# Kernel tuning notes

Hardware: AMD Instinct MI355X
Metric: run time of the kernel (lower is better)

Reference implementation:

```python
import jax, jax.numpy as jnp
import numpy as np

N_GRIDS, N_FEATS = 64, 2
GD = GH = GW = 64
PE_TERMS, N_DIMS = 6, 3
NODES, N_OUT = 64, 1
N_PTS = 524288


def setup_inputs() -> dict:
    key = jax.random.key(0)
    ks = jax.random.split(key, 8)
    x = jax.random.uniform(ks[0], (N_PTS, N_DIMS), jnp.float32, -1.0, 1.0)
    grid_scales = jax.random.uniform(ks[1], (N_GRIDS, 3), jnp.float32, 1.0, 4.0)
    grid_translations = jax.random.uniform(ks[2], (N_GRIDS, 3), jnp.float32, -1.0, 1.0) * (grid_scales - 1.0)
    feature_grids = jax.random.normal(ks[3], (N_GRIDS, N_FEATS, GD, GH, GW), jnp.float32)
    d_in = PE_TERMS * N_DIMS * 2 + N_FEATS * N_GRIDS  # 36 + 128 = 164
    W0 = jax.random.normal(ks[4], (d_in, NODES), jnp.float32) * np.sqrt(2.0 / (d_in + NODES))
    b0 = jnp.zeros((NODES,), jnp.float32)
    W1 = jax.random.normal(ks[5], (NODES, NODES), jnp.float32) * np.sqrt(2.0 / (2 * NODES))
    b1 = jnp.zeros((NODES,), jnp.float32)
    W2 = jax.random.normal(ks[6], (NODES, N_OUT), jnp.float32) * np.sqrt(2.0 / (NODES + N_OUT))
    b2 = jnp.zeros((N_OUT,), jnp.float32)
    return dict(x=x, grid_scales=grid_scales, grid_translations=grid_translations,
                feature_grids=feature_grids, W0=W0, b0=b0, W1=W1, b1=b1, W2=W2, b2=b2)


def grid_sample_3d(vol, coords):
    """Trilinear grid_sample, align_corners=True, padding_mode='zeros'.
    vol: [C,D,H,W]; coords: [N,3] in (x,y,z) order (x -> W axis), range [-1,1].
    Returns [C,N]."""
    C, D, H, W = vol.shape
    flat = vol.reshape(C, D * H * W)
    ix = (coords[:, 0] + 1.0) * 0.5 * (W - 1)
    iy = (coords[:, 1] + 1.0) * 0.5 * (H - 1)
    iz = (coords[:, 2] + 1.0) * 0.5 * (D - 1)
    x0 = jnp.floor(ix); y0 = jnp.floor(iy); z0 = jnp.floor(iz)
    wx = ix - x0; wy = iy - y0; wz = iz - z0
    x0i = x0.astype(jnp.int32); y0i = y0.astype(jnp.int32); z0i = z0.astype(jnp.int32)
    out = jnp.zeros((C, coords.shape[0]), vol.dtype)
    for dz, wz_ in ((0, 1.0 - wz), (1, wz)):
        for dy, wy_ in ((0, 1.0 - wy), (1, wy)):
            for dx, wx_ in ((0, 1.0 - wx), (1, wx)):
                xi = x0i + dx; yi = y0i + dy; zi = z0i + dz
                valid = (xi >= 0) & (xi < W) & (yi >= 0) & (yi < H) & (zi >= 0) & (zi < D)
                idx = (jnp.clip(zi, 0, D - 1) * H + jnp.clip(yi, 0, H - 1)) * W + jnp.clip(xi, 0, W - 1)
                v = jnp.take(flat, idx, axis=1) * valid.astype(vol.dtype)[None, :]
                out = out + v * (wz_ * wy_ * wx_)[None, :]
    return out


def positional_encoding(x):
    # NeRF-style PE: sin/cos of pi*2^i * x, i in [0, PE_TERMS), out dim = 2*L*3
    freqs = jnp.pi * (2.0 ** jnp.arange(PE_TERMS, dtype=jnp.float32))  # [L]
    ang = x[:, None, :] * freqs[None, :, None]                          # [N,L,3]
    n = x.shape[0]
    return jnp.concatenate([jnp.sin(ang).reshape(n, -1), jnp.cos(ang).reshape(n, -1)], axis=1)


def snake_alt(x):
    return 0.5 * x + jnp.sin(x) ** 2


def reference(x, grid_scales, grid_translations, feature_grids, W0, b0, W1, b1, W2, b2):
    # per-grid affine transform (equivalent to bmm with the scale+translation 4x4)
    tp = x[None, :, :] * grid_scales[:, None, :] + grid_translations[:, None, :]  # [G,N,3]
    feats = jax.vmap(grid_sample_3d)(feature_grids, tp)  # [G,C,N]
    G, C, N = feats.shape
    feats = feats.reshape(G * C, N).T                    # [N, G*C]
    pe = positional_encoding(x)                          # [N, 2*L*3]
    y = jnp.concatenate([pe, feats], axis=1)
    y = snake_alt(y @ W0 + b0)
    y = snake_alt(y @ W1 + b1)
    y = y @ W2 + b2
    return y
```

## Files before the change

kernel.cpp:

```cpp
#include <hip/hip_runtime.h>
#include <hip/hip_bf16.h>

#define NPTS    524288
#define NG      64
#define GSZ     64
#define VOX     (GSZ*GSZ*GSZ)
#define NODES   64
#define TILE    64
#define NBLK    (NPTS / TILE)
#define K0      192
#define SF      200
#define NCELL   4096
#define PREP_VB 16384
#define PREP_CB 2048

typedef __attribute__((ext_vector_type(8))) short bf16x8;
typedef __attribute__((ext_vector_type(4))) float f32x4;

__device__ inline unsigned short f2bf(float f) {
    __hip_bfloat16 b = __float2bfloat16(f);
    union { __hip_bfloat16 h; unsigned short u; } cv; cv.h = b;
    return cv.u;
}
__device__ inline unsigned int pk2(float c0, float c1) {
    return (unsigned int)f2bf(c0) | ((unsigned int)f2bf(c1) << 16);
}
__device__ inline float bflo(unsigned int v) { return __uint_as_float(v << 16); }
__device__ inline float bfhi(unsigned int v) { return __uint_as_float(v & 0xffff0000u); }

__device__ inline int spread4(int v) {
    return (v & 1) | ((v & 2) << 2) | ((v & 4) << 4) | ((v & 8) << 6);
}
__device__ inline int cell_of(float px, float py, float pz) {
    int cx = min(max((int)((px + 1.0f) * 8.0f), 0), 15);
    int cy = min(max((int)((py + 1.0f) * 8.0f), 0), 15);
    int cz = min(max((int)((pz + 1.0f) * 8.0f), 0), 15);
    return spread4(cx) | (spread4(cy) << 1) | (spread4(cz) << 2);
}


__global__ void prep_fused(const float* __restrict__ fg, uint4* __restrict__ vox4,
                           const float* __restrict__ x, unsigned short* __restrict__ cid,
                           int* __restrict__ hist,
                           const float* __restrict__ W0, const float* __restrict__ W1,
                           unsigned short* __restrict__ w0f, unsigned short* __restrict__ w1f) {
    int b = blockIdx.x;
    int tid = threadIdx.x;
    if (b < PREP_VB) {
        int idx = b * 256 + tid;
        int g = idx >> 16;
        int hb = idx & 65535;
        int brick = hb >> 1;
        int h = hb & 1;
        int bx = brick & 31, by = (brick >> 5) & 31, bz = brick >> 10;
        int xx = bx << 1, yy = by << 1, zz = (bz << 1) + h;
        const float* c0 = fg + (size_t)g * (2 * VOX) + ((zz << 6) + yy) * 64 + xx;
        const float* c1 = c0 + VOX;
        float2 a0 = *(const float2*)c0;
        float2 a1 = *(const float2*)(c0 + 64);
        float2 d0 = *(const float2*)c1;
        float2 d1 = *(const float2*)(c1 + 64);
        vox4[idx] = make_uint4(pk2(a0.x, d0.x), pk2(a0.y, d0.y),
                               pk2(a1.x, d1.x), pk2(a1.y, d1.y));
    } else if (b < PREP_VB + PREP_CB) {
        int p = (b - PREP_VB) * 256 + tid;
        int c = cell_of(x[p * 3 + 0], x[p * 3 + 1], x[p * 3 + 2]);
        cid[p] = (unsigned short)c;
        atomicAdd(&hist[c], 1);
    } else {
        int t = (b - PREP_VB - PREP_CB) * 256 + tid;
        for (int i = t; i < 24 * 512; i += 4096) {
            int j = i & 7, ln = (i >> 3) & 63, fi = i >> 9;
            int ks = fi >> 2, nt = fi & 3;
            int k = ks * 32 + ((ln >> 4) << 3) + j, n = nt * 16 + (ln & 15);
            w0f[i] = (k < 164) ? f2bf(W0[k * NODES + n]) : (unsigned short)0;
        }
        {
            int i = t;
            int j = i & 7, ln = (i >> 3) & 63, fi = i >> 9;
            int ks = fi >> 2, nt = fi & 3;
            int k = ks * 32 + ((ln >> 4) << 3) + j, n = nt * 16 + (ln & 15);
            w1f[i] = f2bf(W1[k * NODES + n]);
        }
    }
}

__global__ void sort_scan(const int* __restrict__ hist, int* __restrict__ offs) {
    __shared__ int partial[256];
    int t = threadIdx.x;
    int loc[16];
    int s = 0;
    #pragma unroll
    for (int i = 0; i < 16; ++i) { loc[i] = s; s += hist[t * 16 + i]; }
    partial[t] = s;
    __syncthreads();
    for (int d = 1; d < 256; d <<= 1) {
        int v = (t >= d) ? partial[t - d] : 0;
        __syncthreads();
        partial[t] += v;
        __syncthreads();
    }
    int base = partial[t] - s;
    #pragma unroll
    for (int i = 0; i < 16; ++i) offs[t * 16 + i] = base + loc[i];
}

__global__ void sort_scatter(const float* __restrict__ x, const unsigned short* __restrict__ cell_id,
                             int* __restrict__ offs, float4* __restrict__ spts) {
    int p = blockIdx.x * blockDim.x + threadIdx.x;
    int c = cell_id[p];
    int pos = atomicAdd(&offs[c], 1);
    spts[pos] = make_float4(x[p * 3 + 0], x[p * 3 + 1], x[p * 3 + 2], __int_as_float(p));
}

struct GP {
    int xp0, xp1, yp0, yp1, zp0, zp1;
    float wx0, wx1, wy0, wy1, wz0, wz1;
    const unsigned int* vg;
};
__device__ inline GP gprep(int g, float ix, float iy, float iz,
                           const unsigned int* __restrict__ vox) {
    GP p;
    float fx = floorf(ix), fy = floorf(iy), fz = floorf(iz);
    int x0 = (int)fx, y0 = (int)fy, z0 = (int)fz;
    float wx = ix - fx, wy = iy - fy, wz = iz - fz;
    p.wx0 = (x0 >= 0) ? (1.0f - wx) : 0.0f;
    p.wx1 = (x0 < 63) ? wx : 0.0f;
    p.wy0 = (y0 >= 0) ? (1.0f - wy) : 0.0f;
    p.wy1 = (y0 < 63) ? wy : 0.0f;
    p.wz0 = (z0 >= 0) ? (1.0f - wz) : 0.0f;
    p.wz1 = (z0 < 63) ? wz : 0.0f;
    int xc0 = max(x0, 0), xc1 = min(x0 + 1, 63);
    int yc0 = max(y0, 0), yc1 = min(y0 + 1, 63);
    int zc0 = max(z0, 0), zc1 = min(z0 + 1, 63);
    p.xp0 = ((xc0 >> 1) << 3) | (xc0 & 1);
    p.xp1 = ((xc1 >> 1) << 3) | (xc1 & 1);
    p.yp0 = ((yc0 >> 1) << 8) | ((yc0 & 1) << 1);
    p.yp1 = ((yc1 >> 1) << 8) | ((yc1 & 1) << 1);
    p.zp0 = ((zc0 >> 1) << 13) | ((zc0 & 1) << 2);
    p.zp1 = ((zc1 >> 1) << 13) | ((zc1 & 1) << 2);
    p.vg = vox + ((size_t)g << 18);
    return p;
}

__device__ inline void gather2(int pt, int gA, float axi, float ayi, float azi, bool wrA,
                               int gB, float bxi, float byi, float bzi, bool wrB,
                               const unsigned int* __restrict__ vox,
                               unsigned short* Fsh) {
    GP a = gprep(gA, axi, ayi, azi, vox);
    GP b = gprep(gB, bxi, byi, bzi, vox);
    unsigned int a00 = a.vg[a.zp0 + a.yp0 + a.xp0], a01 = a.vg[a.zp0 + a.yp0 + a.xp1];
    unsigned int a10 = a.vg[a.zp0 + a.yp1 + a.xp0], a11 = a.vg[a.zp0 + a.yp1 + a.xp1];
    unsigned int a20 = a.vg[a.zp1 + a.yp0 + a.xp0], a21 = a.vg[a.zp1 + a.yp0 + a.xp1];
    unsigned int a30 = a.vg[a.zp1 + a.yp1 + a.xp0], a31 = a.vg[a.zp1 + a.yp1 + a.xp1];
    unsigned int b00 = b.vg[b.zp0 + b.yp0 + b.xp0], b01 = b.vg[b.zp0 + b.yp0 + b.xp1];
    unsigned int b10 = b.vg[b.zp0 + b.yp1 + b.xp0], b11 = b.vg[b.zp0 + b.yp1 + b.xp1];
    unsigned int b20 = b.vg[b.zp1 + b.yp0 + b.xp0], b21 = b.vg[b.zp1 + b.yp0 + b.xp1];
    unsigned int b30 = b.vg[b.zp1 + b.yp1 + b.xp0], b31 = b.vg[b.zp1 + b.yp1 + b.xp1];
    {
        float f0 = 0.f, f1 = 0.f, wzy;
        wzy = a.wz0 * a.wy0;
        f0 += wzy * (a.wx0 * bflo(a00) + a.wx1 * bflo(a01));
        f1 += wzy * (a.wx0 * bfhi(a00) + a.wx1 * bfhi(a01));
        wzy = a.wz0 * a.wy1;
        f0 += wzy * (a.wx0 * bflo(a10) + a.wx1 * bflo(a11));
        f1 += wzy * (a.wx0 * bfhi(a10) + a.wx1 * bfhi(a11));
        wzy = a.wz1 * a.wy0;
        f0 += wzy * (a.wx0 * bflo(a20) + a.wx1 * bflo(a21));
        f1 += wzy * (a.wx0 * bfhi(a20) + a.wx1 * bfhi(a21));
        wzy = a.wz1 * a.wy1;
        f0 += wzy * (a.wx0 * bflo(a30) + a.wx1 * bflo(a31));
        f1 += wzy * (a.wx0 * bfhi(a30) + a.wx1 * bfhi(a31));
        if (wrA) *(unsigned int*)&Fsh[pt * SF + 36 + 2 * gA] = pk2(f0, f1);
    }
    {
        float f0 = 0.f, f1 = 0.f, wzy;
        wzy = b.wz0 * b.wy0;
        f0 += wzy * (b.wx0 * bflo(b00) + b.wx1 * bflo(b01));
        f1 += wzy * (b.wx0 * bfhi(b00) + b.wx1 * bfhi(b01));
        wzy = b.wz0 * b.wy1;
        f0 += wzy * (b.wx0 * bflo(b10) + b.wx1 * bflo(b11));
        f1 += wzy * (b.wx0 * bfhi(b10) + b.wx1 * bfhi(b11));
        wzy = b.wz1 * b.wy0;
        f0 += wzy * (b.wx0 * bflo(b20) + b.wx1 * bflo(b21));
        f1 += wzy * (b.wx0 * bfhi(b20) + b.wx1 * bfhi(b21));
        wzy = b.wz1 * b.wy1;
        f0 += wzy * (b.wx0 * bflo(b30) + b.wx1 * bflo(b31));
        f1 += wzy * (b.wx0 * bfhi(b30) + b.wx1 * bfhi(b31));
        if (wrB) *(unsigned int*)&Fsh[pt * SF + 36 + 2 * gB] = pk2(f0, f1);
    }
}

__device__ inline void gather1(int pt, int g, float ix, float iy, float iz, bool wr,
                               const unsigned int* __restrict__ vox,
                               unsigned short* Fsh) {
    GP a = gprep(g, ix, iy, iz, vox);
    unsigned int a00 = a.vg[a.zp0 + a.yp0 + a.xp0], a01 = a.vg[a.zp0 + a.yp0 + a.xp1];
    unsigned int a10 = a.vg[a.zp0 + a.yp1 + a.xp0], a11 = a.vg[a.zp0 + a.yp1 + a.xp1];
    unsigned int a20 = a.vg[a.zp1 + a.yp0 + a.xp0], a21 = a.vg[a.zp1 + a.yp0 + a.xp1];
    unsigned int a30 = a.vg[a.zp1 + a.yp1 + a.xp0], a31 = a.vg[a.zp1 + a.yp1 + a.xp1];
    float f0 = 0.f, f1 = 0.f, wzy;
    wzy = a.wz0 * a.wy0;
    f0 += wzy * (a.wx0 * bflo(a00) + a.wx1 * bflo(a01));
    f1 += wzy * (a.wx0 * bfhi(a00) + a.wx1 * bfhi(a01));
    wzy = a.wz0 * a.wy1;
    f0 += wzy * (a.wx0 * bflo(a10) + a.wx1 * bflo(a11));
    f1 += wzy * (a.wx0 * bfhi(a10) + a.wx1 * bfhi(a11));
    wzy = a.wz1 * a.wy0;
    f0 += wzy * (a.wx0 * bflo(a20) + a.wx1 * bflo(a21));
    f1 += wzy * (a.wx0 * bfhi(a20) + a.wx1 * bfhi(a21));
    wzy = a.wz1 * a.wy1;
    f0 += wzy * (a.wx0 * bflo(a30) + a.wx1 * bflo(a31));
    f1 += wzy * (a.wx0 * bfhi(a30) + a.wx1 * bfhi(a31));
    if (wr) *(unsigned int*)&Fsh[pt * SF + 36 + 2 * g] = pk2(f0, f1);
}

#define EXTRACT(gv, pv) \
    if (mf) { gv = (int)__builtin_ctzll(mf); mf &= mf - 1; pv = false; } \
    else if (mp) { gv = (int)__builtin_ctzll(mp); mp &= mp - 1; pv = true; } \
    else { gv = 0; pv = true; }

__global__ void __launch_bounds__(256, 6)
amrsrn_main(const float4* __restrict__ spts,
            const float* __restrict__ gscale,
            const float* __restrict__ gtrans,
            const unsigned int* __restrict__ vox,
            const unsigned short* __restrict__ w0f,
            const unsigned short* __restrict__ w1f,
            const float* __restrict__ b0,
            const float* __restrict__ b1,
            const float* __restrict__ W2,
            const float* __restrict__ b2,
            float* __restrict__ out) {
    __shared__ unsigned short Fsh[TILE * SF];

    const int tid = threadIdx.x;
    const int lane = tid & 63;
    const int wv = tid >> 6;
    const int cb = ((blockIdx.x & 7) << 10) | (blockIdx.x >> 3);
    const int base = cb * TILE;
    const int ptb = wv * 16;
    const int ptloc = lane >> 2;
    const int sub = lane & 3;
    const int pt = ptb + ptloc;

    float4 sp = spts[base + pt];
    const float px = sp.x, py = sp.y, pz = sp.z;
    const int sreg = __float_as_int(sp.w);

    {
        uint4* zp = (uint4*)(Fsh + ptb * SF);
        for (int i = lane; i < 16 * SF / 8; i += 64) zp[i] = make_uint4(0, 0, 0, 0);
    }

    #pragma unroll
    for (int t = 0; t < 9; ++t) {
        int tau = sub * 9 + t;
        int tt = (tau < 18) ? tau : tau - 18;
        int l = tt / 3, d = tt - l * 3;
        float c = (d == 0) ? px : ((d == 1) ? py : pz);
        float ang = c * (3.14159265358979323846f * (float)(1 << l));
        float val = (tau < 18) ? __sinf(ang) : __cosf(ang);
        Fsh[pt * SF + tau] = f2bf(val);
    }

    float lox = px, hix = px, loy = py, hiy = py, loz = pz, hiz = pz;
    #pragma unroll
    for (int m = 1; m < 64; m <<= 1) {
        lox = fminf(lox, __shfl_xor(lox, m)); hix = fmaxf(hix, __shfl_xor(hix, m));
        loy = fminf(loy, __shfl_xor(loy, m)); hiy = fmaxf(hiy, __shfl_xor(hiy, m));
        loz = fminf(loz, __shfl_xor(loz, m)); hiz = fmaxf(hiz, __shfl_xor(hiz, m));
    }
    unsigned long long mf, mp;
    {
        int g = lane;
        float s0 = gscale[g*3+0], s1 = gscale[g*3+1], s2 = gscale[g*3+2];
        float t0 = gtrans[g*3+0], t1 = gtrans[g*3+1], t2 = gtrans[g*3+2];
        float xl = (lox*s0 + t0 + 1.0f)*31.5f, xh = (hix*s0 + t0 + 1.0f)*31.5f;
        float yl = (loy*s1 + t1 + 1.0f)*31.5f, yh = (hiy*s1 + t1 + 1.0f)*31.5f;
        float zl = (loz*s2 + t2 + 1.0f)*31.5f, zh = (hiz*s2 + t2 + 1.0f)*31.5f;
        bool fullg = (xl >= -0.999f) & (xh <= 63.999f)
                   & (yl >= -0.999f) & (yh <= 63.999f)
                   & (zl >= -0.999f) & (zh <= 63.999f);
        bool outg  = (xh < -1.001f) | (xl >= 64.001f)
                   | (yh < -1.001f) | (yl >= 64.001f)
                   | (zh < -1.001f) | (zl >= 64.001f);
        mf = __ballot(fullg);
        mp = __ballot(!fullg && !outg);
    }

    {
        int total = __popcll(mf) + __popcll(mp);
        int done = 0;
        while (done < total) {
            int g0,g1,g2,g3,g4,g5,g6,g7; bool p0,p1,p2,p3,p4,p5,p6,p7;
            EXTRACT(g0,p0) EXTRACT(g1,p1) EXTRACT(g2,p2) EXTRACT(g3,p3)
            EXTRACT(g4,p4) EXTRACT(g5,p5) EXTRACT(g6,p6) EXTRACT(g7,p7)
            int  gA = sub==0?g0: sub==1?g1: sub==2?g2:g3;
            bool pA = sub==0?p0: sub==1?p1: sub==2?p2:p3;
            bool avA = (done + sub) < total;
            float ixA = (px * gscale[gA*3+0] + gtrans[gA*3+0] + 1.0f) * 31.5f;
            float iyA = (py * gscale[gA*3+1] + gtrans[gA*3+1] + 1.0f) * 31.5f;
            float izA = (pz * gscale[gA*3+2] + gtrans[gA*3+2] + 1.0f) * 31.5f;
            bool wrA = avA && (!pA || ((ixA >= -1.0f) & (ixA < 64.0f)
                                     & (iyA >= -1.0f) & (iyA < 64.0f)
                                     & (izA >= -1.0f) & (izA < 64.0f)));
            if (done + 4 < total) {
                int  gB = sub==0?g4: sub==1?g5: sub==2?g6:g7;
                bool pB = sub==0?p4: sub==1?p5: sub==2?p6:p7;
                bool avB = (done + 4 + sub) < total;
                float ixB = (px * gscale[gB*3+0] + gtrans[gB*3+0] + 1.0f) * 31.5f;
                float iyB = (py * gscale[gB*3+1] + gtrans[gB*3+1] + 1.0f) * 31.5f;
                float izB = (pz * gscale[gB*3+2] + gtrans[gB*3+2] + 1.0f) * 31.5f;
                bool wrB = avB && (!pB || ((ixB >= -1.0f) & (ixB < 64.0f)
                                         & (iyB >= -1.0f) & (iyB < 64.0f)
                                         & (izB >= -1.0f) & (izB < 64.0f)));
                gather2(pt, gA, ixA, iyA, izA, wrA, gB, ixB, iyB, izB, wrB, vox, Fsh);
            } else {
                gather1(pt, gA, ixA, iyA, izA, wrA, vox, Fsh);
            }
            done += 8;
        }
    }

    const int row = lane & 15;
    const int quad = lane >> 4;

    f32x4 acc0[4] = {{0,0,0,0},{0,0,0,0},{0,0,0,0},{0,0,0,0}};
    #pragma unroll
    for (int ks = 0; ks < 6; ++ks) {
        bf16x8 a = *(const bf16x8*)&Fsh[(ptb + row) * SF + ks * 32 + quad * 8];
        #pragma unroll
        for (int nt = 0; nt < 4; ++nt) {
            bf16x8 b = *(const bf16x8*)&w0f[(((ks << 2) + nt) << 9) + (lane << 3)];
            acc0[nt] = __builtin_amdgcn_mfma_f32_16x16x32_bf16(a, b, acc0[nt], 0, 0, 0);
        }
    }
    #pragma unroll
    for (int nt = 0; nt < 4; ++nt) {
        int node = nt * 16 + row;
        float bb = b0[node];
        #pragma unroll
        for (int r = 0; r < 4; ++r) {
            float h = acc0[nt][r] + bb;
            float s = __sinf(h);
            h = 0.5f * h + s * s;
            Fsh[(ptb + quad * 4 + r) * SF + node] = f2bf(h);
        }
    }

    f32x4 acc1[4] = {{0,0,0,0},{0,0,0,0},{0,0,0,0},{0,0,0,0}};
    #pragma unroll
    for (int ks = 0; ks < 2; ++ks) {
        bf16x8 a = *(const bf16x8*)&Fsh[(ptb + row) * SF + ks * 32 + quad * 8];
        #pragma unroll
        for (int nt = 0; nt < 4; ++nt) {
            bf16x8 b = *(const bf16x8*)&w1f[(((ks << 2) + nt) << 9) + (lane << 3)];
            acc1[nt] = __builtin_amdgcn_mfma_f32_16x16x32_bf16(a, b, acc1[nt], 0, 0, 0);
        }
    }
    float part[4] = {0.f, 0.f, 0.f, 0.f};
    #pragma unroll
    for (int nt = 0; nt < 4; ++nt) {
        int node = nt * 16 + row;
        float b1v = b1[node];
        float w2v = W2[node];
        #pragma unroll
        for (int r = 0; r < 4; ++r) {
            float h = acc1[nt][r] + b1v;
            float s = __sinf(h);
            h = 0.5f * h + s * s;
            part[r] += h * w2v;
        }
    }
    #pragma unroll
    for (int m = 1; m < 16; m <<= 1) {
        #pragma unroll
        for (int r = 0; r < 4; ++r) part[r] += __shfl_xor(part[r], m);
    }
    int o0 = __shfl(sreg, (quad * 4 + 0) << 2);
    int o1 = __shfl(sreg, (quad * 4 + 1) << 2);
    int o2 = __shfl(sreg, (quad * 4 + 2) << 2);
    int o3 = __shfl(sreg, (quad * 4 + 3) << 2);
    if (row == 0) {
        float b2v = b2[0];
        out[o0] = part[0] + b2v;
        out[o1] = part[1] + b2v;
        out[o2] = part[2] + b2v;
        out[o3] = part[3] + b2v;
    }
}

__global__ void amrsrn_fallback(const float* __restrict__ x,
                                const float* __restrict__ gscale,
                                const float* __restrict__ gtrans,
                                const float* __restrict__ fg,
                                const float* __restrict__ W0,
                                const float* __restrict__ b0,
                                const float* __restrict__ W1,
                                const float* __restrict__ b1,
                                const float* __restrict__ W2,
                                const float* __restrict__ b2,
                                float* __restrict__ out) {
    int p = blockIdx.x * blockDim.x + threadIdx.x;
    float px = x[p*3+0], py = x[p*3+1], pz = x[p*3+2];
    float h0[NODES];
    #pragma unroll
    for (int j = 0; j < NODES; ++j) h0[j] = b0[j];
    #pragma unroll
    for (int l = 0; l < 6; ++l) {
        float freq = 3.14159265358979323846f * (float)(1 << l);
        #pragma unroll
        for (int d = 0; d < 3; ++d) {
            float v = (d == 0 ? px : (d == 1 ? py : pz)) * freq;
            float s = __sinf(v), c = __cosf(v);
            const float* wrs = W0 + (l*3 + d) * NODES;
            const float* wrc = W0 + (18 + l*3 + d) * NODES;
            #pragma unroll
            for (int j = 0; j < NODES; ++j) h0[j] += s * wrs[j] + c * wrc[j];
        }
    }
    for (int g = 0; g < NG; ++g) {
        float ix = (px * gscale[g*3+0] + gtrans[g*3+0] + 1.0f) * 31.5f;
        float iy = (py * gscale[g*3+1] + gtrans[g*3+1] + 1.0f) * 31.5f;
        float iz = (pz * gscale[g*3+2] + gtrans[g*3+2] + 1.0f) * 31.5f;
        float fxf = floorf(ix), fyf = floorf(iy), fzf = floorf(iz);
        int x0 = (int)fxf, y0 = (int)fyf, z0 = (int)fzf;
        float wx = ix - fxf, wy = iy - fyf, wz = iz - fzf;
        bool any = (x0 >= -1 && x0 < GSZ) && (y0 >= -1 && y0 < GSZ) && (z0 >= -1 && z0 < GSZ);
        if (any) {
            float f0 = 0.f, f1 = 0.f;
            #pragma unroll
            for (int dz = 0; dz < 2; ++dz) {
                int zi = z0 + dz; bool vz = ((unsigned)zi < (unsigned)GSZ);
                int zc = min(max(zi, 0), GSZ - 1);
                float wzf = dz ? wz : 1.f - wz;
                #pragma unroll
                for (int dy = 0; dy < 2; ++dy) {
                    int yi = y0 + dy; bool vy = ((unsigned)yi < (unsigned)GSZ);
                    int yc = min(max(yi, 0), GSZ - 1);
                    float wyf = dy ? wy : 1.f - wy;
                    int rowoff = (zc * GSZ + yc) * GSZ;
                    #pragma unroll
                    for (int dx = 0; dx < 2; ++dx) {
                        int xi = x0 + dx; bool vx = ((unsigned)xi < (unsigned)GSZ);
                        int xc = min(max(xi, 0), GSZ - 1);
                        float w = wzf * wyf * (dx ? wx : 1.f - wx);
                        w = (vz && vy && vx) ? w : 0.f;
                        const float* gp = fg + ((size_t)g << 19);
                        f0 += w * gp[rowoff + xc];
                        f1 += w * gp[VOX + rowoff + xc];
                    }
                }
            }
            const float* wr = W0 + (36 + 2*g) * NODES;
            #pragma unroll
            for (int j = 0; j < NODES; ++j) h0[j] += f0 * wr[j] + f1 * wr[NODES + j];
        }
    }
    #pragma unroll
    for (int j = 0; j < NODES; ++j) { float s = __sinf(h0[j]); h0[j] = 0.5f * h0[j] + s * s; }
    float out_acc = b2[0];
    #pragma unroll
    for (int half = 0; half < 2; ++half) {
        float h1[32];
        #pragma unroll
        for (int j = 0; j < 32; ++j) h1[j] = b1[half*32 + j];
        #pragma unroll
        for (int i = 0; i < NODES; ++i) {
            float a = h0[i];
            const float* w1r = W1 + i * NODES + half*32;
            #pragma unroll
            for (int j = 0; j < 32; ++j) h1[j] += a * w1r[j];
        }
        #pragma unroll
        for (int j = 0; j < 32; ++j) { float s = __sinf(h1[j]); out_acc += (0.5f * h1[j] + s * s) * W2[half*32 + j]; }
    }
    out[p] = out_acc;
}

extern "C" void kernel_launch(void* const* d_in, const int* in_sizes, int n_in,
                              void* d_out, int out_size, void* d_ws, size_t ws_size,
                              hipStream_t stream) {
    const float* x      = (const float*)d_in[0];
    const float* gscale = (const float*)d_in[1];
    const float* gtrans = (const float*)d_in[2];
    const float* fg     = (const float*)d_in[3];
    const float* W0     = (const float*)d_in[4];
    const float* b0     = (const float*)d_in[5];
    const float* W1     = (const float*)d_in[6];
    const float* b1     = (const float*)d_in[7];
    const float* W2     = (const float*)d_in[8];
    const float* b2     = (const float*)d_in[9];
    float* out = (float*)d_out;

    char* wsp = (char*)d_ws;
    unsigned short* w0f = (unsigned short*)wsp;
    unsigned short* w1f = w0f + 24 * 512;
    int* hist           = (int*)(wsp + (64 << 10));
    int* offs           = (int*)(wsp + (80 << 10));
    unsigned short* cid = (unsigned short*)(wsp + (96 << 10));
    float4* spts        = (float4*)(wsp + (96 << 10) + (1 << 20));
    unsigned int* vox   = (unsigned int*)(wsp + (96 << 10) + (1 << 20) + (8 << 20));
    const size_t ws_needed = (96 << 10) + (1 << 20) + (8 << 20) + (size_t)NG * VOX * 4;

    if (ws_size >= ws_needed) {
        hipMemsetAsync(hist, 0, NCELL * sizeof(int), stream);
        prep_fused<<<PREP_VB + PREP_CB + 16, 256, 0, stream>>>(
            fg, (uint4*)vox, x, cid, hist, W0, W1, w0f, w1f);
        sort_scan<<<1, 256, 0, stream>>>(hist, offs);
        sort_scatter<<<NPTS / 256, 256, 0, stream>>>(x, cid, offs, spts);
        amrsrn_main<<<NBLK, 256, 0, stream>>>(spts, gscale, gtrans, vox,
                                              w0f, w1f, b0, b1, W2, b2, out);
    } else {
        amrsrn_fallback<<<NPTS / 256, 256, 0, stream>>>(
            x, gscale, gtrans, fg, W0, b0, W1, b1, W2, b2, out);
    }
}
```

Before: 395.4 us.

## Software-pipeline grid gathers with double-buffered stages and lower occupancy bound

Restructures the trilinear gather loop into a two-stage software pipeline. The voxel loads for the next pair of grids are issued before the interpolation of the current pair is computed and written to shared memory. This hides global-memory gather latency behind arithmetic. In exchange it holds many more live registers, so the launch bound drops from 6 to 5 waves per SIMD, and it skips the loads and weights entirely when a sample is invalid.

After: 392.4 us. About the same (-0.7%).

```diff
diff --git a/kernel.cpp b/kernel.cpp
--- a/kernel.cpp
+++ b/kernel.cpp
@@ -113,106 +113,73 @@
     spts[pos] = make_float4(x[p * 3 + 0], x[p * 3 + 1], x[p * 3 + 2], __int_as_float(p));
 }
 
-struct GP {
-    int xp0, xp1, yp0, yp1, zp0, zp1;
-    float wx0, wx1, wy0, wy1, wz0, wz1;
-    const unsigned int* vg;
+struct StageG {
+    unsigned int c00, c01, c10, c11, c20, c21, c30, c31;
+    float zy00, zy01, zy10, zy11, x0w, x1w;
+    int col;
+    bool wr;
 };
-__device__ inline GP gprep(int g, float ix, float iy, float iz,
-                           const unsigned int* __restrict__ vox) {
-    GP p;
-    float fx = floorf(ix), fy = floorf(iy), fz = floorf(iz);
-    int x0 = (int)fx, y0 = (int)fy, z0 = (int)fz;
-    float wx = ix - fx, wy = iy - fy, wz = iz - fz;
-    p.wx0 = (x0 >= 0) ? (1.0f - wx) : 0.0f;
-    p.wx1 = (x0 < 63) ? wx : 0.0f;
-    p.wy0 = (y0 >= 0) ? (1.0f - wy) : 0.0f;
-    p.wy1 = (y0 < 63) ? wy : 0.0f;
-    p.wz0 = (z0 >= 0) ? (1.0f - wz) : 0.0f;
-    p.wz1 = (z0 < 63) ? wz : 0.0f;
-    int xc0 = max(x0, 0), xc1 = min(x0 + 1, 63);
-    int yc0 = max(y0, 0), yc1 = min(y0 + 1, 63);
-    int zc0 = max(z0, 0), zc1 = min(z0 + 1, 63);
-    p.xp0 = ((xc0 >> 1) << 3) | (xc0 & 1);
-    p.xp1 = ((xc1 >> 1) << 3) | (xc1 & 1);
-    p.yp0 = ((yc0 >> 1) << 8) | ((yc0 & 1) << 1);
-    p.yp1 = ((yc1 >> 1) << 8) | ((yc1 & 1) << 1);
-    p.zp0 = ((zc0 >> 1) << 13) | ((zc0 & 1) << 2);
-    p.zp1 = ((zc1 >> 1) << 13) | ((zc1 & 1) << 2);
-    p.vg = vox + ((size_t)g << 18);
-    return p;
-}
-
-__device__ inline void gather2(int pt, int gA, float axi, float ayi, float azi, bool wrA,
-                               int gB, float bxi, float byi, float bzi, bool wrB,
-                               const unsigned int* __restrict__ vox,
-                               unsigned short* Fsh) {
-    GP a = gprep(gA, axi, ayi, azi, vox);
-    GP b = gprep(gB, bxi, byi, bzi, vox);
-    unsigned int a00 = a.vg[a.zp0 + a.yp0 + a.xp0], a01 = a.vg[a.zp0 + a.yp0 + a.xp1];
-    unsigned int a10 = a.vg[a.zp0 + a.yp1 + a.xp0], a11 = a.vg[a.zp0 + a.yp1 + a.xp1];
-    unsigned int a20 = a.vg[a.zp1 + a.yp0 + a.xp0], a21 = a.vg[a.zp1 + a.yp0 + a.xp1];
-    unsigned int a30 = a.vg[a.zp1 + a.yp1 + a.xp0], a31 = a.vg[a.zp1 + a.yp1 + a.xp1];
-    unsigned int b00 = b.vg[b.zp0 + b.yp0 + b.xp0], b01 = b.vg[b.zp0 + b.yp0 + b.xp1];
-    unsigned int b10 = b.vg[b.zp0 + b.yp1 + b.xp0], b11 = b.vg[b.zp0 + b.yp1 + b.xp1];
-    unsigned int b20 = b.vg[b.zp1 + b.yp0 + b.xp0], b21 = b.vg[b.zp1 + b.yp0 + b.xp1];
-    unsigned int b30 = b.vg[b.zp1 + b.yp1 + b.xp0], b31 = b.vg[b.zp1 + b.yp1 + b.xp1];
-    {
-        float f0 = 0.f, f1 = 0.f, wzy;
-        wzy = a.wz0 * a.wy0;
-        f0 += wzy * (a.wx0 * bflo(a00) + a.wx1 * bflo(a01));
-        f1 += wzy * (a.wx0 * bfhi(a00) + a.wx1 * bfhi(a01));
-        wzy = a.wz0 * a.wy1;
-        f0 += wzy * (a.wx0 * bflo(a10) + a.wx1 * bflo(a11));
-        f1 += wzy * (a.wx0 * bfhi(a10) + a.wx1 * bfhi(a11));
-        wzy = a.wz1 * a.wy0;
-        f0 += wzy * (a.wx0 * bflo(a20) + a.wx1 * bflo(a21));
-        f1 += wzy * (a.wx0 * bfhi(a20) + a.wx1 * bfhi(a21));
-        wzy = a.wz1 * a.wy1;
-        f0 += wzy * (a.wx0 * bflo(a30) + a.wx1 * bflo(a31));
-        f1 += wzy * (a.wx0 * bfhi(a30) + a.wx1 * bfhi(a31));
-        if (wrA) *(unsigned int*)&Fsh[pt * SF + 36 + 2 * gA] = pk2(f0, f1);
-    }
-    {
-        float f0 = 0.f, f1 = 0.f, wzy;
-        wzy = b.wz0 * b.wy0;
-        f0 += wzy * (b.wx0 * bflo(b00) + b.wx1 * bflo(b01));
-        f1 += wzy * (b.wx0 * bfhi(b00) + b.wx1 * bfhi(b01));
-        wzy = b.wz0 * b.wy1;
-        f0 += wzy * (b.wx0 * bflo(b10) + b.wx1 * bflo(b11));
-        f1 += wzy * (b.wx0 * bfhi(b10) + b.wx1 * bfhi(b11));
-        wzy = b.wz1 * b.wy0;
-        f0 += wzy * (b.wx0 * bflo(b20) + b.wx1 * bflo(b21));
-        f1 += wzy * (b.wx0 * bfhi(b20) + b.wx1 * bfhi(b21));
-        wzy = b.wz1 * b.wy1;
-        f0 += wzy * (b.wx0 * bflo(b30) + b.wx1 * bflo(b31));
-        f1 += wzy * (b.wx0 * bfhi(b30) + b.wx1 * bfhi(b31));
-        if (wrB) *(unsigned int*)&Fsh[pt * SF + 36 + 2 * gB] = pk2(f0, f1);
-    }
-}
-
-__device__ inline void gather1(int pt, int g, float ix, float iy, float iz, bool wr,
-                               const unsigned int* __restrict__ vox,
-                               unsigned short* Fsh) {
-    GP a = gprep(g, ix, iy, iz, vox);
-    unsigned int a00 = a.vg[a.zp0 + a.yp0 + a.xp0], a01 = a.vg[a.zp0 + a.yp0 + a.xp1];
-    unsigned int a10 = a.vg[a.zp0 + a.yp1 + a.xp0], a11 = a.vg[a.zp0 + a.yp1 + a.xp1];
-    unsigned int a20 = a.vg[a.zp1 + a.yp0 + a.xp0], a21 = a.vg[a.zp1 + a.yp0 + a.xp1];
-    unsigned int a30 = a.vg[a.zp1 + a.yp1 + a.xp0], a31 = a.vg[a.zp1 + a.yp1 + a.xp1];
-    float f0 = 0.f, f1 = 0.f, wzy;
-    wzy = a.wz0 * a.wy0;
-    f0 += wzy * (a.wx0 * bflo(a00) + a.wx1 * bflo(a01));
-    f1 += wzy * (a.wx0 * bfhi(a00) + a.wx1 * bfhi(a01));
-    wzy = a.wz0 * a.wy1;
-    f0 += wzy * (a.wx0 * bflo(a10) + a.wx1 * bflo(a11));
-    f1 += wzy * (a.wx0 * bfhi(a10) + a.wx1 * bfhi(a11));
-    wzy = a.wz1 * a.wy0;
-    f0 += wzy * (a.wx0 * bflo(a20) + a.wx1 * bflo(a21));
-    f1 += wzy * (a.wx0 * bfhi(a20) + a.wx1 * bfhi(a21));
-    wzy = a.wz1 * a.wy1;
-    f0 += wzy * (a.wx0 * bflo(a30) + a.wx1 * bflo(a31));
-    f1 += wzy * (a.wx0 * bfhi(a30) + a.wx1 * bfhi(a31));
-    if (wr) *(unsigned int*)&Fsh[pt * SF + 36 + 2 * g] = pk2(f0, f1);
+
+__device__ __forceinline__ void issue_one(int g, bool part, bool avail,
+                                          float px, float py, float pz,
+                                          const float* __restrict__ gscale,
+                                          const float* __restrict__ gtrans,
+                                          const unsigned int* __restrict__ vox,
+                                          int ptSF, StageG &S) {
+    S.wr = false;
+    if (avail) {
+        float ix = (px * gscale[g*3+0] + gtrans[g*3+0] + 1.0f) * 31.5f;
+        float iy = (py * gscale[g*3+1] + gtrans[g*3+1] + 1.0f) * 31.5f;
+        float iz = (pz * gscale[g*3+2] + gtrans[g*3+2] + 1.0f) * 31.5f;
+        bool ok = !part || ((ix >= -1.0f) & (ix < 64.0f)
+                          & (iy >= -1.0f) & (iy < 64.0f)
+                          & (iz >= -1.0f) & (iz < 64.0f));
+        if (ok) {
+            float fx = floorf(ix), fy = floorf(iy), fz = floorf(iz);
+            int x0 = (int)fx, y0 = (int)fy, z0 = (int)fz;
+            float wx = ix - fx, wy = iy - fy, wz = iz - fz;
+            float wx0 = (x0 >= 0) ? (1.0f - wx) : 0.0f;
+            float wx1 = (x0 < 63) ? wx : 0.0f;
+            float wy0 = (y0 >= 0) ? (1.0f - wy) : 0.0f;
+            float wy1 = (y0 < 63) ? wy : 0.0f;
+            float wz0 = (z0 >= 0) ? (1.0f - wz) : 0.0f;
+            float wz1 = (z0 < 63) ? wz : 0.0f;
+            int xc0 = max(x0, 0), xc1 = min(x0 + 1, 63);
+            int yc0 = max(y0, 0), yc1 = min(y0 + 1, 63);
+            int zc0 = max(z0, 0), zc1 = min(z0 + 1, 63);
+            int xp0 = ((xc0 >> 1) << 3) | (xc0 & 1);
+            int xp1 = ((xc1 >> 1) << 3) | (xc1 & 1);
+            int yp0 = ((yc0 >> 1) << 8) | ((yc0 & 1) << 1);
+            int yp1 = ((yc1 >> 1) << 8) | ((yc1 & 1) << 1);
+            int zp0 = ((zc0 >> 1) << 13) | ((zc0 & 1) << 2);
+            int zp1 = ((zc1 >> 1) << 13) | ((zc1 & 1) << 2);
+            const unsigned int* vg = vox + ((size_t)g << 18);
+            S.c00 = vg[zp0 + yp0 + xp0]; S.c01 = vg[zp0 + yp0 + xp1];
+            S.c10 = vg[zp0 + yp1 + xp0]; S.c11 = vg[zp0 + yp1 + xp1];
+            S.c20 = vg[zp1 + yp0 + xp0]; S.c21 = vg[zp1 + yp0 + xp1];
+            S.c30 = vg[zp1 + yp1 + xp0]; S.c31 = vg[zp1 + yp1 + xp1];
+            S.zy00 = wz0 * wy0; S.zy01 = wz0 * wy1;
+            S.zy10 = wz1 * wy0; S.zy11 = wz1 * wy1;
+            S.x0w = wx0; S.x1w = wx1;
+            S.col = ptSF + 36 + 2 * g;
+            S.wr = true;
+        }
+    }
+}
+
+__device__ __forceinline__ void tree_one(const StageG &S, unsigned short* Fsh) {
+    if (S.wr) {
+        float f0 = 0.f, f1 = 0.f;
+        f0 += S.zy00 * (S.x0w * bflo(S.c00) + S.x1w * bflo(S.c01));
+        f1 += S.zy00 * (S.x0w * bfhi(S.c00) + S.x1w * bfhi(S.c01));
+        f0 += S.zy01 * (S.x0w * bflo(S.c10) + S.x1w * bflo(S.c11));
+        f1 += S.zy01 * (S.x0w * bfhi(S.c10) + S.x1w * bfhi(S.c11));
+        f0 += S.zy10 * (S.x0w * bflo(S.c20) + S.x1w * bflo(S.c21));
+        f1 += S.zy10 * (S.x0w * bfhi(S.c20) + S.x1w * bfhi(S.c21));
+        f0 += S.zy11 * (S.x0w * bflo(S.c30) + S.x1w * bflo(S.c31));
+        f1 += S.zy11 * (S.x0w * bfhi(S.c30) + S.x1w * bfhi(S.c31));
+        *(unsigned int*)&Fsh[S.col] = pk2(f0, f1);
+    }
 }
 
 #define EXTRACT(gv, pv) \
@@ -220,7 +187,25 @@
     else if (mp) { gv = (int)__builtin_ctzll(mp); mp &= mp - 1; pv = true; } \
     else { gv = 0; pv = true; }
 
-__global__ void __launch_bounds__(256, 6)
+__device__ __forceinline__ void stage_issue(unsigned long long &mf, unsigned long long &mp,
+                                            int done, int total, int sub,
+                                            float px, float py, float pz,
+                                            const float* __restrict__ gscale,
+                                            const float* __restrict__ gtrans,
+                                            const unsigned int* __restrict__ vox,
+                                            int ptSF, StageG &A, StageG &B) {
+    int g0,g1,g2,g3,g4,g5,g6,g7; bool p0,p1,p2,p3,p4,p5,p6,p7;
+    EXTRACT(g0,p0) EXTRACT(g1,p1) EXTRACT(g2,p2) EXTRACT(g3,p3)
+    EXTRACT(g4,p4) EXTRACT(g5,p5) EXTRACT(g6,p6) EXTRACT(g7,p7)
+    int  gA = sub==0?g0: sub==1?g1: sub==2?g2:g3;
+    bool pA = sub==0?p0: sub==1?p1: sub==2?p2:p3;
+    int  gB = sub==0?g4: sub==1?g5: sub==2?g6:g7;
+    bool pB = sub==0?p4: sub==1?p5: sub==2?p6:p7;
+    issue_one(gA, pA, (done + sub) < total,     px, py, pz, gscale, gtrans, vox, ptSF, A);
+    issue_one(gB, pB, (done + 4 + sub) < total, px, py, pz, gscale, gtrans, vox, ptSF, B);
+}
+
+__global__ void __launch_bounds__(256, 5)
 amrsrn_main(const float4* __restrict__ spts,
             const float* __restrict__ gscale,
             const float* __restrict__ gtrans,
@@ -292,34 +277,27 @@
     {
         int total = __popcll(mf) + __popcll(mp);
         int done = 0;
-        while (done < total) {
-            int g0,g1,g2,g3,g4,g5,g6,g7; bool p0,p1,p2,p3,p4,p5,p6,p7;
-            EXTRACT(g0,p0) EXTRACT(g1,p1) EXTRACT(g2,p2) EXTRACT(g3,p3)
-            EXTRACT(g4,p4) EXTRACT(g5,p5) EXTRACT(g6,p6) EXTRACT(g7,p7)
-            int  gA = sub==0?g0: sub==1?g1: sub==2?g2:g3;
-            bool pA = sub==0?p0: sub==1?p1: sub==2?p2:p3;
-            bool avA = (done + sub) < total;
-            float ixA = (px * gscale[gA*3+0] + gtrans[gA*3+0] + 1.0f) * 31.5f;
-            float iyA = (py * gscale[gA*3+1] + gtrans[gA*3+1] + 1.0f) * 31.5f;
-            float izA = (pz * gscale[gA*3+2] + gtrans[gA*3+2] + 1.0f) * 31.5f;
-            bool wrA = avA && (!pA || ((ixA >= -1.0f) & (ixA < 64.0f)
-                                     & (iyA >= -1.0f) & (iyA < 64.0f)
-                                     & (izA >= -1.0f) & (izA < 64.0f)));
-            if (done + 4 < total) {
-                int  gB = sub==0?g4: sub==1?g5: sub==2?g6:g7;
-                bool pB = sub==0?p4: sub==1?p5: sub==2?p6:p7;
-                bool avB = (done + 4 + sub) < total;
-                float ixB = (px * gscale[gB*3+0] + gtrans[gB*3+0] + 1.0f) * 31.5f;
-                float iyB = (py * gscale[gB*3+1] + gtrans[gB*3+1] + 1.0f) * 31.5f;
-                float izB = (pz * gscale[gB*3+2] + gtrans[gB*3+2] + 1.0f) * 31.5f;
-                bool wrB = avB && (!pB || ((ixB >= -1.0f) & (ixB < 64.0f)
-                                         & (iyB >= -1.0f) & (iyB < 64.0f)
-                                         & (izB >= -1.0f) & (izB < 64.0f)));
-                gather2(pt, gA, ixA, iyA, izA, wrA, gB, ixB, iyB, izB, wrB, vox, Fsh);
-            } else {
-                gather1(pt, gA, ixA, iyA, izA, wrA, vox, Fsh);
+        const int ptSF = pt * SF;
+        StageG A0, B0, A1, B1;
+        bool h0 = done < total;
+        if (h0) {
+            stage_issue(mf, mp, done, total, sub, px, py, pz, gscale, gtrans, vox, ptSF, A0, B0);
+            done += 8;
+        }
+        while (h0) {
+            bool h1 = done < total;
+            if (h1) {
+                stage_issue(mf, mp, done, total, sub, px, py, pz, gscale, gtrans, vox, ptSF, A1, B1);
+                done += 8;
             }
-            done += 8;
+            tree_one(A0, Fsh); tree_one(B0, Fsh);
+            if (!h1) break;
+            h0 = done < total;
+            if (h0) {
+                stage_issue(mf, mp, done, total, sub, px, py, pz, gscale, gtrans, vox, ptSF, A0, B0);
+                done += 8;
+            }
+            tree_one(A1, Fsh); tree_one(B1, Fsh);
         }
     }
 
```
